# Kernel tuning notes

Hardware: AMD Instinct MI355X
Metric: run time of the kernel (lower is better)

Reference implementation:

```python
import jax, jax.numpy as jnp
import numpy as np
from jax import lax

B, C, H, W = 64, 384, 28, 28
E, K, R = 3, 2, 8          # num_experts, top_k, lora rank
HID = 4 * C                # ConvNeXt MLP hidden
EPS = 1e-6
SCALING = 8.0 / 8.0        # alpha / r


def setup_inputs() -> dict:
    key = jax.random.key(0)
    ks = jax.random.split(key, 18)
    N = B * H * W
    f32 = jnp.float32
    inp = {
        "x": jax.random.normal(ks[0], (B, C, H, W), f32),
        "conv_w": jax.random.normal(ks[1], (C, 1, 7, 7), f32) * 0.05,
        "conv_b": jax.random.normal(ks[2], (C,), f32) * 0.02,
        "norm_g": 1.0 + jax.random.normal(ks[3], (C,), f32) * 0.02,
        "norm_b": jax.random.normal(ks[4], (C,), f32) * 0.02,
        "dom_g": jax.random.normal(ks[5], (E, C), f32) * 0.02,
        "dom_b": jax.random.normal(ks[6], (E, C), f32) * 0.02,
        "fc1_w": jax.random.normal(ks[7], (C, HID), f32) * (C ** -0.5),
        "fc1_b": jax.random.normal(ks[8], (HID,), f32) * 0.02,
        "fc2_w": jax.random.normal(ks[9], (HID, C), f32) * (HID ** -0.5),
        "fc2_b": jax.random.normal(ks[10], (C,), f32) * 0.02,
        "w_down": jax.random.normal(ks[11], (E, C, R), f32) * (C ** -0.5),
        "w_up": jax.random.normal(ks[12], (E, R, C), f32) * 0.02,
        "gamma": jax.random.normal(ks[13], (C,), f32) * 0.1,
        "routing_weights": jax.nn.softmax(jax.random.normal(ks[14], (B, E), f32), axis=-1),
        "topk_probs": jax.nn.softmax(jax.random.normal(ks[15], (N, K), f32), axis=-1),
        "topk_indices": jax.random.randint(ks[16], (N, K), 0, E),
    }
    return inp


def _forward(x, conv_w, conv_b, norm_g, norm_b, dom_g, dom_b,
             fc1_w, fc1_b, fc2_w, fc2_b, w_down, w_up, gamma,
             routing_weights, topk_probs, topk_indices):
    shortcut = x
    # depthwise 7x7 conv, NCHW, SAME padding
    y = lax.conv_general_dilated(
        x, conv_w, window_strides=(1, 1), padding=((3, 3), (3, 3)),
        feature_group_count=C,
        dimension_numbers=("NCHW", "OIHW", "NCHW"))
    y = y + conv_b[None, :, None, None]
    y = jnp.transpose(y, (0, 2, 3, 1))  # [B, H, W, C] channels-last path

    # ParallelMoELayerNorm: orig LN + sum_i w_i * LN_i(x). All LNs share eps,
    # so normalize once and fuse affine params per-sample.
    mu = jnp.mean(y, axis=-1, keepdims=True)
    var = jnp.mean(jnp.square(y - mu), axis=-1, keepdims=True)
    xhat = (y - mu) * lax.rsqrt(var + EPS)
    g_eff = norm_g[None, :] + routing_weights @ dom_g   # [B, C]
    b_eff = norm_b[None, :] + routing_weights @ dom_b   # [B, C]
    y = xhat * g_eff[:, None, None, :] + b_eff[:, None, None, :]

    # base ConvNeXt MLP (exact GELU, as torch nn.GELU)
    h = jax.nn.gelu(jnp.einsum("bhwc,cf->bhwf", y, fc1_w) + fc1_b,
                    approximate=False)
    orig_out = jnp.einsum("bhwf,fc->bhwc", h, fc2_w) + fc2_b

    # MoE LoRA: dense per-expert rank-8 compute, combined with top-k weights.
    # Equivalent math to the gather/matmul/scatter-add loop in the source.
    y_flat = y.reshape(-1, C)                                   # [N, C]
    down = jnp.einsum("nc,ecr->enr", y_flat, w_down)            # [E, N, R]
    up = jnp.einsum("enr,erc->enc", jax.nn.gelu(down, approximate=False), w_up)
    # combine weights: comb[n, e] = sum_k topk_probs[n, k] * (topk_indices[n,k]==e)
    comb = jnp.sum(jax.nn.one_hot(topk_indices, E, dtype=y.dtype)
                   * topk_probs[..., None], axis=1)             # [N, E]
    moe_out = jnp.einsum("enc,ne->nc", up * SCALING, comb)
    y = orig_out + moe_out.reshape(B, H, W, C)

    y = jnp.transpose(y, (0, 3, 1, 2))  # back to NCHW
    y = gamma[None, :, None, None] * y  # layer scale; drop_path = identity (eval)
    return y + shortcut


def reference(x, conv_w, conv_b, norm_g, norm_b, dom_g, dom_b,
              fc1_w, fc1_b, fc2_w, fc2_b, w_down, w_up, gamma,
              routing_weights, topk_probs, topk_indices):
    return _forward(x, conv_w, conv_b, norm_g, norm_b, dom_g, dom_b,
                    fc1_w, fc1_b, fc2_w, fc2_b, w_down, w_up, gamma,
                    routing_weights, topk_probs, topk_indices)
```

## Files before the change

### kernel.cpp

```cpp
#include <hip/hip_runtime.h>
#include <hip/hip_bf16.h>
#include <cstdint>
#include <cstddef>

constexpr int cB   = 64;
constexpr int cC   = 384;
constexpr int cH   = 28;
constexpr int cW   = 28;
constexpr int cHID = 1536;
constexpr int cNTOK = cB * cH * cW;
constexpr int cKP   = cHID + 32;
constexpr int cCH   = 2;
constexpr int cMR   = cNTOK / cCH;

typedef __attribute__((ext_vector_type(8))) short bf16x8;
typedef __attribute__((ext_vector_type(4))) float f32x4;

__device__ __forceinline__ float gelu_f(float x) {
  float u = 1.5957691216057308f * x * (1.0f + 0.044715f * x * x);
  float e = __expf(-u);
  return x / (1.0f + e);
}

__device__ __forceinline__ float bf16_to_f(short s) {
  return __uint_as_float(((unsigned)(unsigned short)s) << 16);
}

__device__ __forceinline__ void gload_lds16(const void* g, void* l) {
  __builtin_amdgcn_global_load_lds(
      (const __attribute__((address_space(1))) unsigned int*)g,
      (__attribute__((address_space(3))) unsigned int*)l, 16, 0, 0);
}

__device__ __forceinline__ int xcd_remap(int b, int nwg) {
  int qn = nwg >> 3, rm = nwg & 7;
  int xcd = b & 7, off = b >> 3;
  return (xcd < rm) ? xcd * (qn + 1) + off
                    : rm * (qn + 1) + (xcd - rm) * qn + off;
}

__global__ __launch_bounds__(256) void prep_eff(
    const float* __restrict__ ng, const float* __restrict__ nb,
    const float* __restrict__ dg, const float* __restrict__ db,
    const float* __restrict__ rw, float* __restrict__ geff, float* __restrict__ beff) {
  int i = blockIdx.x * 256 + threadIdx.x;
  if (i >= cB * cC) return;
  int b = i / cC, c = i - b * cC;
  float g = ng[c], bb = nb[c];
#pragma unroll
  for (int e = 0; e < 3; ++e) {
    float r = rw[b * 3 + e];
    g += r * dg[e * cC + c];
    bb += r * db[e * cC + c];
  }
  geff[i] = g;
  beff[i] = bb;
}

__global__ __launch_bounds__(256) void transpose_bf16(
    const float* __restrict__ w, __hip_bfloat16* __restrict__ wt, int R0, int C0) {
  __shared__ float t[64][65];
  int c0 = blockIdx.x * 64, r0 = blockIdx.y * 64;
  for (int i = threadIdx.x; i < 64 * 64; i += 256) {
    int r = i >> 6, c = i & 63;
    t[r][c] = w[(size_t)(r0 + r) * C0 + c0 + c];
  }
  __syncthreads();
  for (int i = threadIdx.x; i < 64 * 64; i += 256) {
    int c = i >> 6, r = i & 63;
    wt[(size_t)(c0 + c) * R0 + r0 + r] = __float2bfloat16(t[r][c]);
  }
}

__global__ __launch_bounds__(256) void build_fc2t(
    const float* __restrict__ fc2w, const float* __restrict__ wu,
    __hip_bfloat16* __restrict__ fc2t) {
  int i = blockIdx.x * 256 + threadIdx.x;
  if (i >= cC * cKP) return;
  int c = i / cKP, k = i - c * cKP;
  float v = 0.f;
  if (k < cHID) v = fc2w[(size_t)k * cC + c];
  else {
    int j = k - cHID;
    if (j < 24) v = wu[(size_t)(j >> 3) * 8 * cC + (size_t)(j & 7) * cC + c];
  }
  fc2t[i] = __float2bfloat16(v);
}

__global__ __launch_bounds__(256) void build_wdt(
    const float* __restrict__ wd, __hip_bfloat16* __restrict__ wdt) {
  int i = blockIdx.x * 256 + threadIdx.x;
  if (i >= 32 * cC) return;
  int j = i / cC, c = i - j * cC;
  float v = 0.f;
  if (j < 24) v = wd[(size_t)(j >> 3) * cC * 8 + (size_t)c * 8 + (j & 7)];
  wdt[i] = __float2bfloat16(v);
}

constexpr int cPL = 8;
__global__ __launch_bounds__(256) void conv_dw(
    const float* __restrict__ x, const float* __restrict__ cw,
    const float* __restrict__ cb, float* __restrict__ out) {
  int pb = blockIdx.x * cPL;
  int c0 = pb % cC;
  __shared__ __align__(16) float tile[cPL][34][38];
  __shared__ float wsm[cPL][49];
  const int tid = threadIdx.x;

  float2 z2 = {0.f, 0.f};
  for (int i = tid; i < cPL * 34 * 38 / 2; i += 256)
    ((float2*)tile)[i] = z2;
  __syncthreads();

  for (int i = tid; i < cPL * 196; i += 256) {
    int p = i / 196, q = i - p * 196;
    int r = q / 7, cl = (q - r * 7) * 4;
    float4 v = *(const float4*)&x[(size_t)(pb + p) * 784 + r * 28 + cl];
    float* dst = &tile[p][r + 3][cl + 4];
    *(float2*)dst = make_float2(v.x, v.y);
    *(float2*)(dst + 2) = make_float2(v.z, v.w);
  }
  for (int i = tid; i < cPL * 49; i += 256) {
    int p = i / 49, k = i - p * 49;
    wsm[p][k] = cw[(size_t)(c0 + p) * 49 + k];
  }
  __syncthreads();

  if (tid < cPL * 28) {
    int p = tid / 28, r = tid - p * 28;
    float acc[28];
    float cbv = cb[c0 + p];
#pragma unroll
    for (int w = 0; w < 28; ++w) acc[w] = cbv;
    for (int dh = 0; dh < 7; ++dh) {
      float rowv[36];
      const float* rp = &tile[p][r + dh][0];
#pragma unroll
      for (int k = 0; k < 18; ++k)
        ((float2*)rowv)[k] = *(const float2*)(rp + k * 2);
      float w7[7];
#pragma unroll
      for (int dw = 0; dw < 7; ++dw) w7[dw] = wsm[p][dh * 7 + dw];
#pragma unroll
      for (int w = 0; w < 28; ++w)
#pragma unroll
        for (int dw = 0; dw < 7; ++dw)
          acc[w] += rowv[w + dw + 1] * w7[dw];
    }
    float* op = out + (size_t)(pb + p) * 784 + r * 28;
#pragma unroll
    for (int k = 0; k < 7; ++k)
      *(float4*)&op[k * 4] = *(float4*)&acc[k * 4];
  }
}

__global__ __launch_bounds__(256) void ln_affine(
    const float* __restrict__ convout, const float* __restrict__ geff,
    const float* __restrict__ beff, __hip_bfloat16* __restrict__ y) {
  int bh = blockIdx.x;
  int b = bh / cH;
  int hrow = bh - b * cH;
  __shared__ float t[cC * 29];
  const float* src = convout + (size_t)b * cC * (cH * cW) + (size_t)hrow * cW;
  for (int i = threadIdx.x; i < cC * cW; i += 256) {
    int c = i / cW, w = i - c * cW;
    t[c * 29 + w] = src[(size_t)c * (cH * cW) + w];
  }
  __syncthreads();
  int wave = threadIdx.x >> 6, lane = threadIdx.x & 63;
  const float* gp = geff + (size_t)b * cC;
  const float* bp = beff + (size_t)b * cC;
  for (int w = wave; w < cW; w += 4) {
    float v[6], s = 0.f, s2 = 0.f;
#pragma unroll
    for (int j = 0; j < 6; ++j) {
      v[j] = t[(lane + 64 * j) * 29 + w];
      s += v[j];
      s2 += v[j] * v[j];
    }
#pragma unroll
    for (int d = 32; d; d >>= 1) {
      s += __shfl_xor(s, d);
      s2 += __shfl_xor(s2, d);
    }
    float mu = s * (1.0f / cC);
    float var = s2 * (1.0f / cC) - mu * mu;
    float rstd = rsqrtf(var + 1e-6f);
    size_t n = (size_t)bh * cW + w;
#pragma unroll
    for (int j = 0; j < 6; ++j) {
      int c = lane + 64 * j;
      float val = (v[j] - mu) * rstd * gp[c] + bp[c];
      y[n * cC + c] = __float2bfloat16(val);
    }
  }
}

template <int DO_GELU>
__global__ __launch_bounds__(256) void gemm_bt(
    const __hip_bfloat16* __restrict__ A, int lda,
    const __hip_bfloat16* __restrict__ Bt,
    const float* __restrict__ bias,
    __hip_bfloat16* __restrict__ Cb, int ldc,
    int M, int N, int K, int NT_N) {
  __shared__ __align__(16) __hip_bfloat16 As[2][128 * 32];
  __shared__ __align__(16) __hip_bfloat16 Bs[2][128 * 32];

  const int bid = xcd_remap(blockIdx.x, gridDim.x);
  const int gsz = 8 * NT_N;
  const int g = bid / gsz;
  const int q = bid - g * gsz;
  const int mi = g * 8 + q / NT_N;
  const int ni = q - (q / NT_N) * NT_N;
  const int m0 = mi * 128, n0 = ni * 128;

  const int tid = threadIdx.x;
  const int lane = tid & 63;
  const int wid = tid >> 6;
  const int wm = wid >> 1, wn = wid & 1;

  const int base0 = wid * 2048;
  const int base1 = base0 + 1024;
  const int off0 = base0 + lane * 16, off1 = base1 + lane * 16;
  const int row0 = off0 >> 6, col0 = (off0 >> 1) & 31;
  const int row1 = off1 >> 6, col1 = (off1 >> 1) & 31;
  const __hip_bfloat16* pa0 = &A[(size_t)(m0 + row0) * lda + col0];
  const __hip_bfloat16* pa1 = &A[(size_t)(m0 + row1) * lda + col1];
  const __hip_bfloat16* pb0 = &Bt[(size_t)(n0 + row0) * K + col0];
  const __hip_bfloat16* pb1 = &Bt[(size_t)(n0 + row1) * K + col1];

  const int nt = K >> 5;

  gload_lds16(pa0, (char*)As[0] + base0);
  gload_lds16(pa1, (char*)As[0] + base1);
  gload_lds16(pb0, (char*)Bs[0] + base0);
  gload_lds16(pb1, (char*)Bs[0] + base1);
  pa0 += 32; pa1 += 32; pb0 += 32; pb1 += 32;
  __syncthreads();

  f32x4 acc[4][4] = {};
  int cur = 0;
  for (int t = 0; t < nt; ++t, cur ^= 1) {
    if (t + 1 < nt) {
      gload_lds16(pa0, (char*)As[cur ^ 1] + base0);
      gload_lds16(pa1, (char*)As[cur ^ 1] + base1);
      gload_lds16(pb0, (char*)Bs[cur ^ 1] + base0);
      gload_lds16(pb1, (char*)Bs[cur ^ 1] + base1);
      pa0 += 32; pa1 += 32; pb0 += 32; pb1 += 32;
    }
    bf16x8 af[4], bfr[4];
#pragma unroll
    for (int i = 0; i < 4; ++i)
      af[i] = *(const bf16x8*)&As[cur][(wm * 64 + i * 16 + (lane & 15)) * 32 + (lane >> 4) * 8];
#pragma unroll
    for (int i = 0; i < 4; ++i)
      bfr[i] = *(const bf16x8*)&Bs[cur][(wn * 64 + i * 16 + (lane & 15)) * 32 + (lane >> 4) * 8];
#pragma unroll
    for (int i = 0; i < 4; ++i)
#pragma unroll
      for (int j = 0; j < 4; ++j)
        acc[i][j] = __builtin_amdgcn_mfma_f32_16x16x32_bf16(af[i], bfr[j], acc[i][j], 0, 0, 0);
    __syncthreads();
  }

#pragma unroll
  for (int i = 0; i < 4; ++i) {
    int row = m0 + wm * 64 + i * 16 + (lane >> 4) * 4;
#pragma unroll
    for (int j = 0; j < 4; ++j) {
      int col = n0 + wn * 64 + j * 16 + (lane & 15);
      float bv = bias[col];
#pragma unroll
      for (int r = 0; r < 4; ++r) {
        float vv = acc[i][j][r] + bv;
        if (DO_GELU) vv = gelu_f(vv);
        Cb[(size_t)(row + r) * ldc + col] = __float2bfloat16(vv);
      }
    }
  }
}

__global__ __launch_bounds__(256) void lora_down(
    const __hip_bfloat16* __restrict__ y,
    const __hip_bfloat16* __restrict__ wdt,
    const float* __restrict__ probs,
    const int* __restrict__ inds,
    __hip_bfloat16* __restrict__ h) {
  __shared__ __align__(16) __hip_bfloat16 As[2][128 * 32];
  __shared__ __align__(16) __hip_bfloat16 Bsm[32 * 384];
  const int tid = threadIdx.x, lane = tid & 63, wid = tid >> 6;
  const int n0 = blockIdx.x * 128;

  for (int i = tid; i < 32 * 384 / 8; i += 256)
    ((bf16x8*)Bsm)[i] = ((const bf16x8*)wdt)[i];

  const int base0 = wid * 2048, base1 = base0 + 1024;
  const int off0 = base0 + lane * 16, off1 = base1 + lane * 16;
  const int row0 = off0 >> 6, col0 = (off0 >> 1) & 31;
  const int row1 = off1 >> 6, col1 = (off1 >> 1) & 31;
  const __hip_bfloat16* pa0 = &y[(size_t)(n0 + row0) * cC + col0];
  const __hip_bfloat16* pa1 = &y[(size_t)(n0 + row1) * cC + col1];

  const int nt = cC >> 5;
  gload_lds16(pa0, (char*)As[0] + base0);
  gload_lds16(pa1, (char*)As[0] + base1);
  pa0 += 32; pa1 += 32;
  __syncthreads();

  f32x4 acc[2][2] = {};
  int cur = 0;
  for (int t = 0; t < nt; ++t, cur ^= 1) {
    if (t + 1 < nt) {
      gload_lds16(pa0, (char*)As[cur ^ 1] + base0);
      gload_lds16(pa1, (char*)As[cur ^ 1] + base1);
      pa0 += 32; pa1 += 32;
    }
    int kt = t * 32;
    bf16x8 af[2], bfr[2];
#pragma unroll
    for (int i = 0; i < 2; ++i)
      af[i] = *(const bf16x8*)&As[cur][(wid * 32 + i * 16 + (lane & 15)) * 32 + (lane >> 4) * 8];
#pragma unroll
    for (int j = 0; j < 2; ++j)
      bfr[j] = *(const bf16x8*)&Bsm[(j * 16 + (lane & 15)) * 384 + kt + (lane >> 4) * 8];
#pragma unroll
    for (int i = 0; i < 2; ++i)
#pragma unroll
      for (int j = 0; j < 2; ++j)
        acc[i][j] = __builtin_amdgcn_mfma_f32_16x16x32_bf16(af[i], bfr[j], acc[i][j], 0, 0, 0);
    __syncthreads();
  }

#pragma unroll
  for (int i = 0; i < 2; ++i) {
#pragma unroll
    for (int j = 0; j < 2; ++j) {
      int colb = j * 16 + (lane & 15);
#pragma unroll
      for (int r = 0; r < 4; ++r) {
        int n = n0 + wid * 32 + i * 16 + (lane >> 4) * 4 + r;
        float zv = 0.f;
        if (colb < 24) {
          int e = colb >> 3;
          float comb = 0.f;
          if (inds[(size_t)n * 2] == e)     comb += probs[(size_t)n * 2];
          if (inds[(size_t)n * 2 + 1] == e) comb += probs[(size_t)n * 2 + 1];
          zv = comb * gelu_f(acc[i][j][r]);
        }
        h[(size_t)n * cKP + cHID + colb] = __float2bfloat16(zv);
      }
    }
  }
}

__global__ __launch_bounds__(256) void final_out(
    const __hip_bfloat16* __restrict__ tmp, const float* __restrict__ x,
    const float* __restrict__ gamma, float* __restrict__ out) {
  int bh = blockIdx.x;
  int b = bh / cH, hrow = bh - b * cH;
  __shared__ float t[cW * 385];
  const __hip_bfloat16* src = tmp + (size_t)bh * cW * cC;
  for (int i = threadIdx.x; i < cW * cC / 8; i += 256) {
    bf16x8 v = ((const bf16x8*)src)[i];
    int base = i * 8;
    int w = base / cC, c = base - w * cC;
#pragma unroll
    for (int k = 0; k < 8; ++k)
      t[w * 385 + c + k] = bf16_to_f(v[k]);
  }
  __syncthreads();
  const float* xb = x + (size_t)b * cC * (cH * cW) + (size_t)hrow * cW;
  float* ob = out + (size_t)b * cC * (cH * cW) + (size_t)hrow * cW;
  for (int i = threadIdx.x; i < cC * cW; i += 256) {
    int c = i / cW, w = i - c * cW;
    ob[(size_t)c * (cH * cW) + w] = gamma[c] * t[w * 385 + c] + xb[(size_t)c * (cH * cW) + w];
  }
}

extern "C" void kernel_launch(void* const* d_in, const int* in_sizes, int n_in,
                              void* d_out, int out_size, void* d_ws, size_t ws_size,
                              hipStream_t stream) {
  const float* x      = (const float*)d_in[0];
  const float* conv_w = (const float*)d_in[1];
  const float* conv_b = (const float*)d_in[2];
  const float* norm_g = (const float*)d_in[3];
  const float* norm_b = (const float*)d_in[4];
  const float* dom_g  = (const float*)d_in[5];
  const float* dom_b  = (const float*)d_in[6];
  const float* fc1_w  = (const float*)d_in[7];
  const float* fc1_b  = (const float*)d_in[8];
  const float* fc2_w  = (const float*)d_in[9];
  const float* fc2_b  = (const float*)d_in[10];
  const float* w_down = (const float*)d_in[11];
  const float* w_up   = (const float*)d_in[12];
  const float* gamma  = (const float*)d_in[13];
  const float* rw     = (const float*)d_in[14];
  const float* tkp    = (const float*)d_in[15];
  const int*   tki    = (const int*)d_in[16];
  float* out = (float*)d_out;

  char* ws = (char*)d_ws;
  __hip_bfloat16* y      = (__hip_bfloat16*)(ws + 0);
  __hip_bfloat16* tmpb   = (__hip_bfloat16*)(ws + 38535168);
  char*           hslot  = ws + 77070336;
  __hip_bfloat16* h      = (__hip_bfloat16*)hslot;
  float*          convb  = (float*)hslot;
  __hip_bfloat16* fc1t   = (__hip_bfloat16*)(ws + 155746304);
  __hip_bfloat16* fc2t   = (__hip_bfloat16*)(ws + 156925952);
  __hip_bfloat16* wdt    = (__hip_bfloat16*)(ws + 158130176);
  float*          geff   = (float*)(ws + 158154752);
  float*          beff   = (float*)(ws + 158253056);

  prep_eff<<<(cB * cC + 255) / 256, 256, 0, stream>>>(norm_g, norm_b, dom_g, dom_b, rw, geff, beff);
  transpose_bf16<<<dim3(cHID / 64, cC / 64), 256, 0, stream>>>(fc1_w, fc1t, cC, cHID);
  build_fc2t<<<(cC * cKP + 255) / 256, 256, 0, stream>>>(fc2_w, w_up, fc2t);
  build_wdt<<<(32 * cC + 255) / 256, 256, 0, stream>>>(w_down, wdt);
  conv_dw<<<cB * cC / cPL, 256, 0, stream>>>(x, conv_w, conv_b, convb);
  ln_affine<<<cB * cH, 256, 0, stream>>>(convb, geff, beff, y);

  const int NTM = cMR / 128;
  for (int ch = 0; ch < cCH; ++ch) {
    const __hip_bfloat16* ych = y + (size_t)ch * cMR * cC;
    gemm_bt<1><<<NTM * (cHID / 128), 256, 0, stream>>>(
        ych, cC, fc1t, fc1_b, h, cKP, cMR, cHID, cC, cHID / 128);
    lora_down<<<NTM, 256, 0, stream>>>(
        ych, wdt, tkp + (size_t)ch * cMR * 2, tki + (size_t)ch * cMR * 2, h);
    gemm_bt<0><<<NTM * (cC / 128), 256, 0, stream>>>(
        h, cKP, fc2t, fc2_b, tmpb + (size_t)ch * cMR * cC, cC, cMR, cC, cKP, cC / 128);
  }

  final_out<<<cB * cH, 256, 0, stream>>>(tmpb, x, gamma, out);
}
```

Baseline: 430.4 us.

## Store depthwise conv output in bf16 and drop LDS tiling in conv

The depthwise conv kernel is rewritten so each thread handles one output row, reading input rows straight from global memory (relying on cache) instead of staging zero-padded tiles in LDS. Its output is stored as bf16 instead of fp32, and the layernorm kernel reads the bf16 intermediate with vectorized 4-wide loads. This halves the intermediate traffic between the two kernels and removes LDS setup and barriers. It adds an extra bf16 rounding before layernorm and causes redundant global reads of input rows across threads.

```diff
diff --git a/kernel.cpp b/kernel.cpp
--- a/kernel.cpp
+++ b/kernel.cpp
@@ -22,8 +22,12 @@
   return x / (1.0f + e);
 }
 
-__device__ __forceinline__ float bf16_to_f(short s) {
-  return __uint_as_float(((unsigned)(unsigned short)s) << 16);
+__device__ __forceinline__ float bf16_to_f(unsigned short s) {
+  return __uint_as_float(((unsigned)s) << 16);
+}
+__device__ __forceinline__ unsigned short f_to_bf16(float v) {
+  __hip_bfloat16 hb = __float2bfloat16(v);
+  return *reinterpret_cast<unsigned short*>(&hb);
 }
 
 __device__ __forceinline__ void gload_lds16(const void* g, void* l) {
@@ -97,74 +101,70 @@
   wdt[i] = __float2bfloat16(v);
 }
 
-constexpr int cPL = 8;
 __global__ __launch_bounds__(256) void conv_dw(
     const float* __restrict__ x, const float* __restrict__ cw,
-    const float* __restrict__ cb, float* __restrict__ out) {
-  int pb = blockIdx.x * cPL;
-  int c0 = pb % cC;
-  __shared__ __align__(16) float tile[cPL][34][38];
-  __shared__ float wsm[cPL][49];
-  const int tid = threadIdx.x;
-
-  float2 z2 = {0.f, 0.f};
-  for (int i = tid; i < cPL * 34 * 38 / 2; i += 256)
-    ((float2*)tile)[i] = z2;
-  __syncthreads();
-
-  for (int i = tid; i < cPL * 196; i += 256) {
-    int p = i / 196, q = i - p * 196;
-    int r = q / 7, cl = (q - r * 7) * 4;
-    float4 v = *(const float4*)&x[(size_t)(pb + p) * 784 + r * 28 + cl];
-    float* dst = &tile[p][r + 3][cl + 4];
-    *(float2*)dst = make_float2(v.x, v.y);
-    *(float2*)(dst + 2) = make_float2(v.z, v.w);
-  }
-  for (int i = tid; i < cPL * 49; i += 256) {
-    int p = i / 49, k = i - p * 49;
-    wsm[p][k] = cw[(size_t)(c0 + p) * 49 + k];
-  }
-  __syncthreads();
-
-  if (tid < cPL * 28) {
-    int p = tid / 28, r = tid - p * 28;
-    float acc[28];
-    float cbv = cb[c0 + p];
-#pragma unroll
-    for (int w = 0; w < 28; ++w) acc[w] = cbv;
-    for (int dh = 0; dh < 7; ++dh) {
-      float rowv[36];
-      const float* rp = &tile[p][r + dh][0];
-#pragma unroll
-      for (int k = 0; k < 18; ++k)
-        ((float2*)rowv)[k] = *(const float2*)(rp + k * 2);
+    const float* __restrict__ cb, __hip_bfloat16* __restrict__ out) {
+  int gid = blockIdx.x * 256 + threadIdx.x;
+  int plane = gid / cH, r = gid - plane * cH;
+  int c = plane % cC;
+  const float* xp = x + (size_t)plane * (cH * cW);
+  const float* wp = cw + (size_t)c * 49;
+
+  float rowv[36];
+  rowv[0] = rowv[1] = rowv[2] = rowv[3] = 0.f;
+  rowv[32] = rowv[33] = rowv[34] = rowv[35] = 0.f;
+
+  float acc[28];
+  float cbv = cb[c];
+#pragma unroll
+  for (int w = 0; w < 28; ++w) acc[w] = cbv;
+
+  for (int dh = 0; dh < 7; ++dh) {
+    int ir = r + dh - 3;
+    if ((unsigned)ir < (unsigned)cH) {
+      const float4* rp = (const float4*)(xp + ir * 28);
+#pragma unroll
+      for (int k = 0; k < 7; ++k)
+        *(float4*)&rowv[4 + k * 4] = rp[k];
       float w7[7];
 #pragma unroll
-      for (int dw = 0; dw < 7; ++dw) w7[dw] = wsm[p][dh * 7 + dw];
+      for (int dw = 0; dw < 7; ++dw) w7[dw] = wp[dh * 7 + dw];
 #pragma unroll
       for (int w = 0; w < 28; ++w)
 #pragma unroll
         for (int dw = 0; dw < 7; ++dw)
           acc[w] += rowv[w + dw + 1] * w7[dw];
     }
-    float* op = out + (size_t)(pb + p) * 784 + r * 28;
-#pragma unroll
-    for (int k = 0; k < 7; ++k)
-      *(float4*)&op[k * 4] = *(float4*)&acc[k * 4];
+  }
+
+  unsigned short* op = (unsigned short*)out + (size_t)plane * (cH * cW) + r * 28;
+#pragma unroll
+  for (int k = 0; k < 7; ++k) {
+    ushort4 s;
+    s.x = f_to_bf16(acc[k * 4 + 0]);
+    s.y = f_to_bf16(acc[k * 4 + 1]);
+    s.z = f_to_bf16(acc[k * 4 + 2]);
+    s.w = f_to_bf16(acc[k * 4 + 3]);
+    *(ushort4*)&op[k * 4] = s;
   }
 }
 
 __global__ __launch_bounds__(256) void ln_affine(
-    const float* __restrict__ convout, const float* __restrict__ geff,
+    const __hip_bfloat16* __restrict__ convout, const float* __restrict__ geff,
     const float* __restrict__ beff, __hip_bfloat16* __restrict__ y) {
   int bh = blockIdx.x;
   int b = bh / cH;
   int hrow = bh - b * cH;
   __shared__ float t[cC * 29];
-  const float* src = convout + (size_t)b * cC * (cH * cW) + (size_t)hrow * cW;
-  for (int i = threadIdx.x; i < cC * cW; i += 256) {
-    int c = i / cW, w = i - c * cW;
-    t[c * 29 + w] = src[(size_t)c * (cH * cW) + w];
+  const unsigned short* src =
+      (const unsigned short*)convout + (size_t)b * cC * (cH * cW) + (size_t)hrow * cW;
+  for (int i = threadIdx.x; i < cC * 7; i += 256) {
+    int c = i / 7, wq = (i - c * 7) * 4;
+    ushort4 v = *(const ushort4*)&src[(size_t)c * (cH * cW) + wq];
+    t[c * 29 + wq + 0] = bf16_to_f(v.x);
+    t[c * 29 + wq + 1] = bf16_to_f(v.y);
+    t[c * 29 + wq + 2] = bf16_to_f(v.z);
+    t[c * 29 + wq + 3] = bf16_to_f(v.w);
   }
   __syncthreads();
   int wave = threadIdx.x >> 6, lane = threadIdx.x & 63;
@@ -366,7 +366,7 @@
     int w = base / cC, c = base - w * cC;
 #pragma unroll
     for (int k = 0; k < 8; ++k)
-      t[w * 385 + c + k] = bf16_to_f(v[k]);
+      t[w * 385 + c + k] = bf16_to_f((unsigned short)v[k]);
   }
   __syncthreads();
   const float* xb = x + (size_t)b * cC * (cH * cW) + (size_t)hrow * cW;
@@ -404,7 +404,7 @@
   __hip_bfloat16* tmpb   = (__hip_bfloat16*)(ws + 38535168);
   char*           hslot  = ws + 77070336;
   __hip_bfloat16* h      = (__hip_bfloat16*)hslot;
-  float*          convb  = (float*)hslot;
+  __hip_bfloat16* convb  = (__hip_bfloat16*)hslot;
   __hip_bfloat16* fc1t   = (__hip_bfloat16*)(ws + 155746304);
   __hip_bfloat16* fc2t   = (__hip_bfloat16*)(ws + 156925952);
   __hip_bfloat16* wdt    = (__hip_bfloat16*)(ws + 158130176);
@@ -415,7 +415,7 @@
   transpose_bf16<<<dim3(cHID / 64, cC / 64), 256, 0, stream>>>(fc1_w, fc1t, cC, cHID);
   build_fc2t<<<(cC * cKP + 255) / 256, 256, 0, stream>>>(fc2_w, w_up, fc2t);
   build_wdt<<<(32 * cC + 255) / 256, 256, 0, stream>>>(w_down, wdt);
-  conv_dw<<<cB * cC / cPL, 256, 0, stream>>>(x, conv_w, conv_b, convb);
+  conv_dw<<<cB * cC * cH / 256, 256, 0, stream>>>(x, conv_w, conv_b, convb);
   ln_affine<<<cB * cH, 256, 0, stream>>>(convb, geff, beff, y);
 
   const int NTM = cMR / 128;
```

New measurement: 552.1 us. 1.28x slower.
